# Optimization experiments

Hardware: AMD Instinct MI355X
Metric: run time of the kernel (lower is better)

## Reference

```python
import jax, jax.numpy as jnp
import numpy as np

B, L = 1024, 50
H = 512
N_ITEM, N_ENTITY, N_WORD = 50000, 100000, 30000


def setup_inputs() -> dict:
    key = jax.random.key(0)
    ks = jax.random.split(key, 16)
    inp = {
        "item_ids": jax.random.randint(ks[0], (B, L), 0, N_ITEM),
        "item_len": jax.random.randint(ks[1], (B,), 0, 51),
        "entity_ids": jax.random.randint(ks[2], (B, L), 0, N_ENTITY),
        "entity_len": jax.random.randint(ks[3], (B,), 0, 51),
        "word_ids": jax.random.randint(ks[4], (B, L), 0, N_WORD),
        "word_len": jax.random.randint(ks[5], (B,), 0, 51),
        "labels": jax.random.randint(ks[6], (B,), 0, N_ITEM),
        # learned parameters (torch default-ish init scales)
        "item_emb": jax.random.normal(ks[7], (N_ITEM, H), jnp.float32),
        "entity_emb": jax.random.normal(ks[8], (N_ENTITY, H), jnp.float32),
        "word_emb": jax.random.normal(ks[9], (N_WORD, H), jnp.float32),
        "W1": jax.random.normal(ks[10], (H, 4 * H), jnp.float32) / np.sqrt(H),
        "b1": jnp.zeros((4 * H,), jnp.float32),
        "W2": jax.random.normal(ks[11], (4 * H, N_ITEM), jnp.float32) / np.sqrt(4 * H),
        "b2": jnp.zeros((N_ITEM,), jnp.float32),
    }
    return inp


def _masked_mean(table, ids, lens):
    # segment-mean over ragged lists encoded as padded ids + lengths.
    # empty list -> zeros (matches the torch zero-fallback branch).
    mask = (jnp.arange(L)[None, :] < lens[:, None]).astype(table.dtype)  # [B,L]
    emb = table[ids]                                                     # [B,L,H]
    s = jnp.einsum("blh,bl->bh", emb, mask)
    denom = jnp.maximum(lens, 1).astype(table.dtype)[:, None]
    return s / denom


def reference(item_emb, entity_emb, word_emb, W1, b1, W2, b2,
              item_ids, item_len, entity_ids, entity_len,
              word_ids, word_len, labels):
    u = (_masked_mean(item_emb, item_ids, item_len)
         + _masked_mean(entity_emb, entity_ids, entity_len)
         + _masked_mean(word_emb, word_ids, word_len)) / 3.0   # [B,H]
    h = jax.nn.relu(u @ W1 + b1)                                # [B,4H]
    probs = jax.nn.softmax(h @ W2 + b2, axis=-1)                # [B,n_item]
    # faithful to source: CrossEntropyLoss applied on top of softmax outputs
    logp = jax.nn.log_softmax(probs, axis=-1)
    loss = -jnp.mean(jnp.take_along_axis(logp, labels[:, None], axis=-1))
    return probs, labels, loss
```

## Files before the change

### kernel.cpp

```cpp
#include <hip/hip_runtime.h>
#include <cstdint>
#include <cstddef>

typedef __attribute__((ext_vector_type(8))) short bf16x8;
typedef __attribute__((ext_vector_type(4))) float f32x4;

#define B_DIM 1024
#define L_SEQ 50
#define H_DIM 512
#define NITEM 50000
#define PSTRIDE 400

__device__ __forceinline__ unsigned short f2bf(float x) {
  unsigned u = __float_as_uint(x);
  return (unsigned short)((u + 0x7fffu + ((u >> 16) & 1u)) >> 16);
}
__device__ __forceinline__ unsigned pack2(float lo, float hi) {
  return (unsigned)f2bf(lo) | ((unsigned)f2bf(hi) << 16);
}
__device__ __forceinline__ void gld16(const unsigned short* g, unsigned short* l) {
  __builtin_amdgcn_global_load_lds((const __attribute__((address_space(1))) void*)g,
                                   (__attribute__((address_space(3))) void*)l, 16, 0, 0);
}

__global__ void mean_kernel(const int* __restrict__ item_ids, const int* __restrict__ item_len,
                            const int* __restrict__ ent_ids, const int* __restrict__ ent_len,
                            const int* __restrict__ word_ids, const int* __restrict__ word_len,
                            const float* __restrict__ item_emb, const float* __restrict__ ent_emb,
                            const float* __restrict__ word_emb, unsigned short* __restrict__ u_bf) {
  const int b = blockIdx.x >> 1;
  const int col = ((blockIdx.x & 1) << 8) + threadIdx.x;
  float out = 0.f;
  {
    const int len = item_len[b]; float a = 0.f;
#pragma unroll 4
    for (int l = 0; l < len; ++l) a += item_emb[(size_t)item_ids[b * L_SEQ + l] * H_DIM + col];
    out += a / (float)(len > 0 ? len : 1);
  }
  {
    const int len = ent_len[b]; float a = 0.f;
#pragma unroll 4
    for (int l = 0; l < len; ++l) a += ent_emb[(size_t)ent_ids[b * L_SEQ + l] * H_DIM + col];
    out += a / (float)(len > 0 ? len : 1);
  }
  {
    const int len = word_len[b]; float a = 0.f;
#pragma unroll 4
    for (int l = 0; l < len; ++l) a += word_emb[(size_t)word_ids[b * L_SEQ + l] * H_DIM + col];
    out += a / (float)(len > 0 ? len : 1);
  }
  u_bf[b * H_DIM + col] = f2bf(out / 3.f);
}

template <int K, int N>
__global__ void transpose_bf16(const float* __restrict__ W, unsigned short* __restrict__ Wt) {
  __shared__ float tile[64][65];
  const int k0 = blockIdx.x * 64, n0 = blockIdx.y * 64;
  const int tn = threadIdx.x & 63, tk = threadIdx.x >> 6;
  const int nv = (n0 + tn < N) ? n0 + tn : N - 1;
#pragma unroll
  for (int i = 0; i < 16; ++i)
    tile[tk + 4 * i][tn] = W[(size_t)(k0 + tk + 4 * i) * N + nv];
  __syncthreads();
  const int rn = threadIdx.x >> 2, ck = (threadIdx.x & 3) * 16;
  if (n0 + rn < N) {
    uint4 o[2];
    unsigned* po = (unsigned*)&o[0];
#pragma unroll
    for (int c = 0; c < 8; ++c)
      po[c] = pack2(tile[ck + 2 * c][rn], tile[ck + 2 * c + 1][rn]);
    *(uint4*)&Wt[(size_t)(n0 + rn) * K + k0 + ck] = o[0];
    *(uint4*)&Wt[(size_t)(n0 + rn) * K + k0 + ck + 8] = o[1];
  }
}

template <int K, int N, int EPI>
__global__ __launch_bounds__(512, 2) void gemm_tt(const unsigned short* __restrict__ Ag,
                                                  const unsigned short* __restrict__ Btg,
                                                  const float* __restrict__ bias,
                                                  unsigned short* __restrict__ Cbf,
                                                  float* __restrict__ Cf,
                                                  float* __restrict__ pmax,
                                                  float* __restrict__ psum) {
  __shared__ unsigned short lds[4][2][256 * 32];

  const int tid = threadIdx.x;
  const int lane = tid & 63;
  const int wid = tid >> 6;

  const int nwg = gridDim.x;
  const int xcd = blockIdx.x & 7, off = blockIdx.x >> 3;
  const int q = nwg >> 3, r = nwg & 7;
  const int wgid = (xcd < r ? xcd * (q + 1) : r * (q + 1) + (xcd - r) * q) + off;
  const int m0 = (wgid & 3) * 256;
  const int bn = wgid >> 2;
  const int n0 = bn * 256;

  const int srow = wid * 16 + (lane >> 2);
  const int schunk = lane & 3;
  const unsigned short* pa[2];
  const unsigned short* pb[2];
  unsigned short* da[2];
  unsigned short* db[2];
#pragma unroll
  for (int L = 0; L < 2; ++L) {
    const int row = L * 128 + srow;
    const int cg = schunk ^ ((row >> 1) & 3);
    pa[L] = Ag + (size_t)(m0 + row) * K + cg * 8;
    int rg = n0 + row;
    rg = rg < N ? rg : N - 1;
    pb[L] = Btg + (size_t)rg * K + cg * 8;
    da[L] = &lds[0][0][L * 4096 + wid * 512];
    db[L] = da[L] + 8192;
  }

  auto stage = [&](int t, int s) {
    const int ko = t * 32;
#pragma unroll
    for (int L = 0; L < 2; ++L) gld16(pa[L] + ko, da[L] + s * 16384);
#pragma unroll
    for (int L = 0; L < 2; ++L) gld16(pb[L] + ko, db[L] + s * 16384);
  };

  const int wr = wid >> 2, wc = wid & 3;
  const int l15 = lane & 15, kb = lane >> 4;
  f32x4 acc[8][4] = {};

  auto compute = [&](int s) {
    bf16x8 af[8], bf[4];
#pragma unroll
    for (int i = 0; i < 8; ++i) {
      const int row = wr * 128 + i * 16 + l15;
      const int c = kb ^ ((row >> 1) & 3);
      af[i] = *(const bf16x8*)&lds[s][0][row * 32 + c * 8];
    }
#pragma unroll
    for (int j = 0; j < 4; ++j) {
      const int col = wc * 64 + j * 16 + l15;
      const int c = kb ^ ((col >> 1) & 3);
      bf[j] = *(const bf16x8*)&lds[s][1][col * 32 + c * 8];
    }
    __builtin_amdgcn_s_setprio(1);
#pragma unroll
    for (int i = 0; i < 8; ++i)
#pragma unroll
      for (int j = 0; j < 4; ++j)
        acc[i][j] = __builtin_amdgcn_mfma_f32_16x16x32_bf16(af[i], bf[j], acc[i][j], 0, 0, 0);
    __builtin_amdgcn_s_setprio(0);
  };

  const int NT = K / 32;
  stage(0, 0);
  stage(1, 1);
  asm volatile("s_waitcnt vmcnt(4)" ::: "memory");
  __builtin_amdgcn_sched_barrier(0);
  __builtin_amdgcn_s_barrier();
  __builtin_amdgcn_sched_barrier(0);
  for (int t = 0; t < NT; ++t) {
    if (t + 2 < NT) stage(t + 2, (t + 2) & 3);
    compute(t & 3);
    if (t + 1 < NT) {
      if (t + 2 < NT)
        asm volatile("s_waitcnt vmcnt(4)" ::: "memory");
      else
        asm volatile("s_waitcnt vmcnt(0)" ::: "memory");
      __builtin_amdgcn_sched_barrier(0);
      __builtin_amdgcn_s_barrier();
      __builtin_amdgcn_sched_barrier(0);
    }
  }

  float bv[4];
  bool val[4];
#pragma unroll
  for (int j = 0; j < 4; ++j) {
    const int cg = n0 + wc * 64 + 16 * j + l15;
    val[j] = (cg < N);
    bv[j] = bias[val[j] ? cg : 0];
  }
#pragma unroll
  for (int i = 0; i < 8; ++i) {
    const int rbase = m0 + wr * 128 + 16 * i + 4 * kb;
#pragma unroll
    for (int j = 0; j < 4; ++j) {
      if (val[j]) {
        const int cg = n0 + wc * 64 + 16 * j + l15;
#pragma unroll
        for (int rr = 0; rr < 4; ++rr) {
          const float v = acc[i][j][rr] + bv[j];
          if (EPI == 0)
            Cbf[(size_t)(rbase + rr) * N + cg] = f2bf(v > 0.f ? v : 0.f);
          else
            Cf[(size_t)(rbase + rr) * N + cg] = v;
        }
      }
    }
  }

  if constexpr (EPI == 1) {
    float* redm = (float*)&lds[0][0][0];
    float* reds = redm + 1024;
#pragma unroll
    for (int i = 0; i < 8; ++i) {
#pragma unroll
      for (int rr = 0; rr < 4; ++rr) {
        float mx = -3.0e38f;
#pragma unroll
        for (int j = 0; j < 4; ++j)
          if (val[j]) mx = fmaxf(mx, acc[i][j][rr] + bv[j]);
#pragma unroll
        for (int d = 1; d < 16; d <<= 1) mx = fmaxf(mx, __shfl_xor(mx, d));
        float s = 0.f;
#pragma unroll
        for (int j = 0; j < 4; ++j)
          if (val[j]) s += expf(acc[i][j][rr] + bv[j] - mx);
#pragma unroll
        for (int d = 1; d < 16; d <<= 1) s += __shfl_xor(s, d);
        if (l15 == 0) {
          const int rw = wr * 128 + 16 * i + 4 * kb + rr;
          redm[wc * 256 + rw] = mx;
          reds[wc * 256 + rw] = s;
        }
      }
    }
    __syncthreads();
    if (tid < 256) {
      float mm = redm[tid], ss = reds[tid];
#pragma unroll
      for (int w = 1; w < 4; ++w) {
        const float ma = redm[w * 256 + tid], sa = reds[w * 256 + tid];
        const float nm = fmaxf(mm, ma);
        ss = ss * expf(mm - nm) + sa * expf(ma - nm);
        mm = nm;
      }
      pmax[(size_t)(m0 + tid) * PSTRIDE + bn] = mm;
      psum[(size_t)(m0 + tid) * PSTRIDE + bn] = ss;
    }
  }
}

template <int K, int N, int EPI>
__global__ __launch_bounds__(512, 2) void gemm_fused(const unsigned short* __restrict__ Ag,
                                                     const float* __restrict__ Bg,
                                                     const float* __restrict__ bias,
                                                     unsigned short* __restrict__ Cbf,
                                                     float* __restrict__ Cf,
                                                     float* __restrict__ pmax,
                                                     float* __restrict__ psum) {
  __shared__ unsigned short As[2][256 * 64];
  __shared__ uint4 Bs[2][8 * 128];
  const int tid = threadIdx.x;
  const int lane = tid & 63;
  const int wid = tid >> 6;
  const int m0 = blockIdx.x * 256;
  const int n0 = blockIdx.y * 128;
  const int arow = tid >> 3;
  const int ach = tid & 7;
  const int bn = 2 * lane;
  const int bk = 8 * wid;
  const int bcolg = (n0 + bn < N - 2) ? (n0 + bn) : (N - 2);
  uint4 areg[4];
  float2 breg[8];
  f32x4 acc[4][4] = {};
  auto stage_global = [&](int kt) {
    const int k0 = kt * 64;
#pragma unroll
    for (int qq = 0; qq < 4; ++qq)
      areg[qq] = *(const uint4*)&Ag[(size_t)(m0 + arow + 64 * qq) * K + k0 + 8 * ach];
#pragma unroll
    for (int i = 0; i < 8; ++i) breg[i] = *(const float2*)&Bg[(size_t)(k0 + bk + i) * N + bcolg];
  };
  auto stage_lds = [&](int buf) {
#pragma unroll
    for (int qq = 0; qq < 4; ++qq) {
      const int row = arow + 64 * qq;
      *(uint4*)&As[buf][row * 64 + ((8 * ach) ^ ((row & 7) * 8))] = areg[qq];
    }
    uint4 c0, c1;
    c0.x = pack2(breg[0].x, breg[1].x); c0.y = pack2(breg[2].x, breg[3].x);
    c0.z = pack2(breg[4].x, breg[5].x); c0.w = pack2(breg[6].x, breg[7].x);
    c1.x = pack2(breg[0].y, breg[1].y); c1.y = pack2(breg[2].y, breg[3].y);
    c1.z = pack2(breg[4].y, breg[5].y); c1.w = pack2(breg[6].y, breg[7].y);
    Bs[buf][wid * 128 + bn] = c0;
    Bs[buf][wid * 128 + bn + 1] = c1;
  };
  const int wr = wid & 3, wc = wid >> 2;
  const int mw = 64 * wr, nw = 64 * wc;
  const int l15 = lane & 15, kb = lane >> 4;
  auto compute = [&](int buf) {
#pragma unroll
    for (int koi = 0; koi < 2; ++koi) {
      bf16x8 af[4], bfv[4];
#pragma unroll
      for (int i = 0; i < 4; ++i) {
        const int row = mw + 16 * i + l15;
        af[i] = *(const bf16x8*)&As[buf][row * 64 + ((32 * koi + 8 * kb) ^ ((row & 7) * 8))];
      }
#pragma unroll
      for (int j = 0; j < 4; ++j)
        bfv[j] = *(const bf16x8*)&Bs[buf][(4 * koi + kb) * 128 + nw + 16 * j + l15];
#pragma unroll
      for (int i = 0; i < 4; ++i)
#pragma unroll
        for (int j = 0; j < 4; ++j)
          acc[i][j] = __builtin_amdgcn_mfma_f32_16x16x32_bf16(af[i], bfv[j], acc[i][j], 0, 0, 0);
    }
  };
  const int NT = K / 64;
  stage_global(0);
  stage_lds(0);
  __syncthreads();
  for (int t = 0; t < NT; ++t) {
    const int cur = t & 1;
    if (t + 1 < NT) stage_global(t + 1);
    compute(cur);
    if (t + 1 < NT) stage_lds(cur ^ 1);
    __syncthreads();
  }
  float bv[4];
  bool val[4];
#pragma unroll
  for (int j = 0; j < 4; ++j) {
    const int cg = n0 + nw + 16 * j + l15;
    val[j] = (cg < N);
    bv[j] = bias[val[j] ? cg : 0];
  }
#pragma unroll
  for (int i = 0; i < 4; ++i) {
    const int rbase = m0 + mw + 16 * i + 4 * kb;
#pragma unroll
    for (int j = 0; j < 4; ++j) {
      if (val[j]) {
        const int cg = n0 + nw + 16 * j + l15;
#pragma unroll
        for (int rr = 0; rr < 4; ++rr) {
          const float v = acc[i][j][rr] + bv[j];
          if (EPI == 0)
            Cbf[(size_t)(rbase + rr) * N + cg] = f2bf(v > 0.f ? v : 0.f);
          else
            Cf[(size_t)(rbase + rr) * N + cg] = v;
        }
      }
    }
  }
  if constexpr (EPI == 1) {
    float* redm = (float*)&As[0][0];
    float* reds = redm + 512;
#pragma unroll
    for (int i = 0; i < 4; ++i) {
#pragma unroll
      for (int rr = 0; rr < 4; ++rr) {
        float mx = -3.0e38f;
#pragma unroll
        for (int j = 0; j < 4; ++j)
          if (val[j]) mx = fmaxf(mx, acc[i][j][rr] + bv[j]);
#pragma unroll
        for (int d = 1; d < 16; d <<= 1) mx = fmaxf(mx, __shfl_xor(mx, d));
        float s = 0.f;
#pragma unroll
        for (int j = 0; j < 4; ++j)
          if (val[j]) s += expf(acc[i][j][rr] + bv[j] - mx);
#pragma unroll
        for (int d = 1; d < 16; d <<= 1) s += __shfl_xor(s, d);
        if (l15 == 0) {
          const int rl = mw + 16 * i + 4 * kb + rr;
          redm[wc * 256 + rl] = mx;
          reds[wc * 256 + rl] = s;
        }
      }
    }
    __syncthreads();
    if (tid < 256) {
      const float ma = redm[tid], mb = redm[256 + tid];
      const float mm = fmaxf(ma, mb);
      const float ss = reds[tid] * expf(ma - mm) + reds[256 + tid] * expf(mb - mm);
      pmax[(size_t)(m0 + tid) * PSTRIDE + blockIdx.y] = mm;
      psum[(size_t)(m0 + tid) * PSTRIDE + blockIdx.y] = ss;
    }
  }
}

__global__ void smax1r(const float* __restrict__ pmax, const float* __restrict__ psum,
                       float* __restrict__ rms, int ntiles) {
  const int b = blockIdx.x;
  const int l = threadIdx.x;
  float m = -3.4e38f, s = 0.f;
  for (int i = l; i < ntiles; i += 64) {
    const float pm = pmax[(size_t)b * PSTRIDE + i];
    const float ps = psum[(size_t)b * PSTRIDE + i];
    const float nm = fmaxf(m, pm);
    s = s * expf(m - nm) + ps * expf(pm - nm);
    m = nm;
  }
  for (int d = 1; d < 64; d <<= 1) {
    const float om = __shfl_xor(m, d), os = __shfl_xor(s, d);
    const float nm = fmaxf(m, om);
    s = s * expf(m - nm) + os * expf(om - nm);
    m = nm;
  }
  if (l == 0) {
    rms[b] = m;
    rms[B_DIM + b] = s;
  }
}

__global__ void smax2(float* __restrict__ buf, const float* __restrict__ rms,
                      const int* __restrict__ labels, float* __restrict__ row_lp) {
  const int b = blockIdx.x;
  float4* p = (float4*)(buf + (size_t)b * NITEM);
  const float m = rms[b];
  const float inv = 1.f / rms[B_DIM + b];
  const int lab = labels[b];
  __shared__ float s_pl;
  __shared__ float ss[256];
  float s2 = 0.f;
  for (int i = threadIdx.x; i < NITEM / 4; i += 256) {
    const float4 v = p[i];
    float pr[4];
#pragma unroll
    for (int j = 0; j < 4; ++j) {
      pr[j] = expf((&v.x)[j] - m) * inv;
      s2 += expf(pr[j] - inv);
    }
    float4 w;
    w.x = pr[0]; w.y = pr[1]; w.z = pr[2]; w.w = pr[3];
    p[i] = w;
    if ((lab >> 2) == i) s_pl = pr[lab & 3];
  }
  ss[threadIdx.x] = s2;
  __syncthreads();
  for (int off = 128; off > 0; off >>= 1) {
    if (threadIdx.x < off) ss[threadIdx.x] += ss[threadIdx.x + off];
    __syncthreads();
  }
  if (threadIdx.x == 0) row_lp[b] = s_pl - (inv + logf(ss[0]));
}

__global__ void fin(const float* __restrict__ row_lp, const int* __restrict__ labels,
                    float* __restrict__ out) {
  __shared__ float sb[256];
  float a = 0.f;
  for (int i = threadIdx.x; i < B_DIM; i += 256) {
    a += row_lp[i];
    out[(size_t)B_DIM * NITEM + i] = (float)labels[i];
  }
  sb[threadIdx.x] = a;
  __syncthreads();
  for (int off = 128; off > 0; off >>= 1) {
    if (threadIdx.x < off) sb[threadIdx.x] += sb[threadIdx.x + off];
    __syncthreads();
  }
  if (threadIdx.x == 0) out[(size_t)B_DIM * NITEM + B_DIM] = -sb[0] / (float)B_DIM;
}

extern "C" void kernel_launch(void* const* d_in, const int* in_sizes, int n_in,
                              void* d_out, int out_size, void* d_ws, size_t ws_size,
                              hipStream_t stream) {
  const int* item_ids = (const int*)d_in[0];
  const int* item_len = (const int*)d_in[1];
  const int* ent_ids = (const int*)d_in[2];
  const int* ent_len = (const int*)d_in[3];
  const int* word_ids = (const int*)d_in[4];
  const int* word_len = (const int*)d_in[5];
  const int* labels = (const int*)d_in[6];
  const float* item_emb = (const float*)d_in[7];
  const float* ent_emb = (const float*)d_in[8];
  const float* word_emb = (const float*)d_in[9];
  const float* W1 = (const float*)d_in[10];
  const float* b1 = (const float*)d_in[11];
  const float* W2 = (const float*)d_in[12];
  const float* b2 = (const float*)d_in[13];

  float* out = (float*)d_out;
  char* ws = (char*)d_ws;
  unsigned short* u_bf = (unsigned short*)ws;
  unsigned short* h_bf = (unsigned short*)(ws + (1 << 20));
  float* pmax = (float*)(ws + 5 * (1 << 20));
  float* psum = (float*)(ws + 7 * (1 << 20));
  float* rms = (float*)(ws + 9 * (1 << 20));
  float* row_lp = rms + 2 * B_DIM;
  unsigned short* W1t = (unsigned short*)(ws + 10 * (1 << 20));
  unsigned short* W2t = (unsigned short*)(ws + 16 * (1 << 20));
  float* logits = out;

  const size_t need = (size_t)16 * (1 << 20) + (size_t)NITEM * 2048 * 2;
  const bool fast = ws_size >= need;

  mean_kernel<<<2 * B_DIM, 256, 0, stream>>>(item_ids, item_len, ent_ids, ent_len, word_ids,
                                             word_len, item_emb, ent_emb, word_emb, u_bf);
  if (fast) {
    transpose_bf16<512, 2048><<<dim3(8, 32), 256, 0, stream>>>(W1, W1t);
    transpose_bf16<2048, NITEM><<<dim3(32, 782), 256, 0, stream>>>(W2, W2t);
    gemm_tt<512, 2048, 0><<<4 * 8, 512, 0, stream>>>(u_bf, W1t, b1, h_bf, nullptr, nullptr,
                                                     nullptr);
    gemm_tt<2048, NITEM, 1><<<4 * 196, 512, 0, stream>>>(h_bf, W2t, b2, nullptr, logits, pmax,
                                                         psum);
    smax1r<<<B_DIM, 64, 0, stream>>>(pmax, psum, rms, 196);
  } else {
    gemm_fused<512, 2048, 0><<<dim3(4, 16), 512, 0, stream>>>(u_bf, W1, b1, h_bf, nullptr,
                                                              nullptr, nullptr);
    gemm_fused<2048, NITEM, 1><<<dim3(4, 391), 512, 0, stream>>>(h_bf, W2, b2, nullptr, logits,
                                                                 pmax, psum);
    smax1r<<<B_DIM, 64, 0, stream>>>(pmax, psum, rms, 391);
  }
  smax2<<<B_DIM, 256, 0, stream>>>(logits, rms, labels, row_lp);
  fin<<<1, 256, 0, stream>>>(row_lp, labels, out);
}
```

Before: 587.8 us.

## Deepen GEMM LDS prefetch to three stages and interleave loads with MFMA halves

Restructures the GEMM main loop to keep three k-tiles in flight in a four-slot LDS ring instead of two. Each iteration is split into two MFMA phases, and the A and B global-to-LDS loads for the stage three tiles ahead are issued between them, separated by extra barriers. The vmcnt waits are recomputed from how many stages are outstanding. This is meant to hide global load latency and spread issue pressure, at the cost of more barriers per iteration and an explicit sync before the softmax reduction reuses LDS.

```diff
diff --git a/kernel.cpp b/kernel.cpp
--- a/kernel.cpp
+++ b/kernel.cpp
@@ -82,7 +82,7 @@
                                                   float* __restrict__ Cf,
                                                   float* __restrict__ pmax,
                                                   float* __restrict__ psum) {
-  __shared__ unsigned short lds[4][2][256 * 32];
+  __shared__ unsigned short lds[4 * 16384];
 
   const int tid = threadIdx.x;
   const int lane = tid & 63;
@@ -100,8 +100,6 @@
   const int schunk = lane & 3;
   const unsigned short* pa[2];
   const unsigned short* pb[2];
-  unsigned short* da[2];
-  unsigned short* db[2];
 #pragma unroll
   for (int L = 0; L < 2; ++L) {
     const int row = L * 128 + srow;
@@ -110,64 +108,86 @@
     int rg = n0 + row;
     rg = rg < N ? rg : N - 1;
     pb[L] = Btg + (size_t)rg * K + cg * 8;
-    da[L] = &lds[0][0][L * 4096 + wid * 512];
-    db[L] = da[L] + 8192;
-  }
-
-  auto stage = [&](int t, int s) {
-    const int ko = t * 32;
-#pragma unroll
-    for (int L = 0; L < 2; ++L) gld16(pa[L] + ko, da[L] + s * 16384);
-#pragma unroll
-    for (int L = 0; L < 2; ++L) gld16(pb[L] + ko, db[L] + s * 16384);
-  };
+  }
 
   const int wr = wid >> 2, wc = wid & 3;
   const int l15 = lane & 15, kb = lane >> 4;
   f32x4 acc[8][4] = {};
 
-  auto compute = [&](int s) {
-    bf16x8 af[8], bf[4];
+  const int NT = K / 32;
+#pragma unroll
+  for (int tt = 0; tt < 3; ++tt) {
+    unsigned short* d = &lds[tt * 16384 + wid * 512];
+    const int ko = tt * 32;
+    gld16(pa[0] + ko, d);
+    gld16(pa[1] + ko, d + 4096);
+    gld16(pb[0] + ko, d + 8192);
+    gld16(pb[1] + ko, d + 12288);
+  }
+  asm volatile("s_waitcnt vmcnt(8)" ::: "memory");
+  asm volatile("s_barrier" ::: "memory");
+
+#pragma unroll 1
+  for (int t = 0; t < NT; ++t) {
+    const unsigned short* As_ = &lds[(t & 3) * 16384];
+    const unsigned short* Bs_ = As_ + 8192;
+    unsigned short* ds_ = &lds[((t + 3) & 3) * 16384 + wid * 512];
+    const int kst = (t + 3) * 32;
+    const bool st = (t + 3) < NT;
+
+    bf16x8 af[8];
 #pragma unroll
     for (int i = 0; i < 8; ++i) {
       const int row = wr * 128 + i * 16 + l15;
-      const int c = kb ^ ((row >> 1) & 3);
-      af[i] = *(const bf16x8*)&lds[s][0][row * 32 + c * 8];
-    }
-#pragma unroll
-    for (int j = 0; j < 4; ++j) {
-      const int col = wc * 64 + j * 16 + l15;
-      const int c = kb ^ ((col >> 1) & 3);
-      bf[j] = *(const bf16x8*)&lds[s][1][col * 32 + c * 8];
-    }
+      af[i] = *(const bf16x8*)&As_[row * 32 + (kb ^ ((row >> 1) & 3)) * 8];
+    }
+    bf16x8 b0, b1;
+    {
+      const int c0 = wc * 64 + l15, c1 = c0 + 16;
+      b0 = *(const bf16x8*)&Bs_[c0 * 32 + (kb ^ ((c0 >> 1) & 3)) * 8];
+      b1 = *(const bf16x8*)&Bs_[c1 * 32 + (kb ^ ((c1 >> 1) & 3)) * 8];
+    }
+    if (st) {
+      gld16(pa[0] + kst, ds_);
+      gld16(pa[1] + kst, ds_ + 4096);
+    }
+    asm volatile("s_barrier" ::: "memory");
     __builtin_amdgcn_s_setprio(1);
 #pragma unroll
-    for (int i = 0; i < 8; ++i)
-#pragma unroll
-      for (int j = 0; j < 4; ++j)
-        acc[i][j] = __builtin_amdgcn_mfma_f32_16x16x32_bf16(af[i], bf[j], acc[i][j], 0, 0, 0);
+    for (int i = 0; i < 8; ++i) {
+      acc[i][0] = __builtin_amdgcn_mfma_f32_16x16x32_bf16(af[i], b0, acc[i][0], 0, 0, 0);
+      acc[i][1] = __builtin_amdgcn_mfma_f32_16x16x32_bf16(af[i], b1, acc[i][1], 0, 0, 0);
+    }
     __builtin_amdgcn_s_setprio(0);
-  };
-
-  const int NT = K / 32;
-  stage(0, 0);
-  stage(1, 1);
-  asm volatile("s_waitcnt vmcnt(4)" ::: "memory");
-  __builtin_amdgcn_sched_barrier(0);
-  __builtin_amdgcn_s_barrier();
-  __builtin_amdgcn_sched_barrier(0);
-  for (int t = 0; t < NT; ++t) {
-    if (t + 2 < NT) stage(t + 2, (t + 2) & 3);
-    compute(t & 3);
-    if (t + 1 < NT) {
-      if (t + 2 < NT)
-        asm volatile("s_waitcnt vmcnt(4)" ::: "memory");
-      else
-        asm volatile("s_waitcnt vmcnt(0)" ::: "memory");
-      __builtin_amdgcn_sched_barrier(0);
-      __builtin_amdgcn_s_barrier();
-      __builtin_amdgcn_sched_barrier(0);
-    }
+    asm volatile("s_barrier" ::: "memory");
+
+    bf16x8 b2, b3;
+    {
+      const int c2 = wc * 64 + 32 + l15, c3 = c2 + 16;
+      b2 = *(const bf16x8*)&Bs_[c2 * 32 + (kb ^ ((c2 >> 1) & 3)) * 8];
+      b3 = *(const bf16x8*)&Bs_[c3 * 32 + (kb ^ ((c3 >> 1) & 3)) * 8];
+    }
+    if (st) {
+      gld16(pb[0] + kst, ds_ + 8192);
+      gld16(pb[1] + kst, ds_ + 12288);
+    }
+    asm volatile("s_barrier" ::: "memory");
+    __builtin_amdgcn_s_setprio(1);
+#pragma unroll
+    for (int i = 0; i < 8; ++i) {
+      acc[i][2] = __builtin_amdgcn_mfma_f32_16x16x32_bf16(af[i], b2, acc[i][2], 0, 0, 0);
+      acc[i][3] = __builtin_amdgcn_mfma_f32_16x16x32_bf16(af[i], b3, acc[i][3], 0, 0, 0);
+    }
+    __builtin_amdgcn_s_setprio(0);
+    const int lim = (t + 3 < NT) ? (t + 3) : (NT - 1);
+    const int ahead = lim - (t + 1);
+    if (ahead >= 2)
+      asm volatile("s_waitcnt vmcnt(8)" ::: "memory");
+    else if (ahead == 1)
+      asm volatile("s_waitcnt vmcnt(4)" ::: "memory");
+    else
+      asm volatile("s_waitcnt vmcnt(0)" ::: "memory");
+    asm volatile("s_barrier" ::: "memory");
   }
 
   float bv[4];
@@ -198,7 +218,8 @@
   }
 
   if constexpr (EPI == 1) {
-    float* redm = (float*)&lds[0][0][0];
+    __syncthreads();
+    float* redm = (float*)&lds[0];
     float* reds = redm + 1024;
 #pragma unroll
     for (int i = 0; i < 8; ++i) {
```

Result: no change. 594.0 us (+1.1%).

## Replace 256x256 four-stage GEMM with 128x128 double-buffered tile kernel

Applied to the files above, without the earlier changes.

Swaps the 256x256-tile, 512-thread GEMM (4-stage LDS pipeline, K-step 32, XCD-aware block remap) for a 128x128-tile, 256-thread kernel with K-step 64, double buffering and a plain 2D grid. The aim is more workgroups and better occupancy and load balance across CUs, since the large GEMM goes from 784 to 3128 blocks. The cost is lower data reuse per tile, roughly double the global/L2 traffic for the operands, a shallower prefetch pipeline, and dropping the XCD locality remap. The softmax partials now cover 391 column blocks instead of 196.

```diff
diff --git a/kernel.cpp b/kernel.cpp
--- a/kernel.cpp
+++ b/kernel.cpp
@@ -75,99 +75,84 @@
 }
 
 template <int K, int N, int EPI>
-__global__ __launch_bounds__(512, 2) void gemm_tt(const unsigned short* __restrict__ Ag,
+__global__ __launch_bounds__(256, 2) void gemm128(const unsigned short* __restrict__ Ag,
                                                   const unsigned short* __restrict__ Btg,
                                                   const float* __restrict__ bias,
                                                   unsigned short* __restrict__ Cbf,
                                                   float* __restrict__ Cf,
                                                   float* __restrict__ pmax,
                                                   float* __restrict__ psum) {
-  __shared__ unsigned short lds[4][2][256 * 32];
+  __shared__ unsigned short As[2][128 * 64];
+  __shared__ unsigned short Bs[2][128 * 64];
 
   const int tid = threadIdx.x;
   const int lane = tid & 63;
   const int wid = tid >> 6;
-
-  const int nwg = gridDim.x;
-  const int xcd = blockIdx.x & 7, off = blockIdx.x >> 3;
-  const int q = nwg >> 3, r = nwg & 7;
-  const int wgid = (xcd < r ? xcd * (q + 1) : r * (q + 1) + (xcd - r) * q) + off;
-  const int m0 = (wgid & 3) * 256;
-  const int bn = wgid >> 2;
-  const int n0 = bn * 256;
-
-  const int srow = wid * 16 + (lane >> 2);
-  const int schunk = lane & 3;
-  const unsigned short* pa[2];
-  const unsigned short* pb[2];
-  unsigned short* da[2];
-  unsigned short* db[2];
-#pragma unroll
-  for (int L = 0; L < 2; ++L) {
-    const int row = L * 128 + srow;
-    const int cg = schunk ^ ((row >> 1) & 3);
-    pa[L] = Ag + (size_t)(m0 + row) * K + cg * 8;
+  const int m0 = blockIdx.x * 128;
+  const int n0 = blockIdx.y * 128;
+
+  const int srsub = lane >> 3;
+  const int scg = (lane & 7) ^ srsub;
+  const unsigned short* pa[4];
+  const unsigned short* pb[4];
+#pragma unroll
+  for (int qq = 0; qq < 4; ++qq) {
+    const int seg = wid * 4 + qq;
+    const int row = seg * 8 + srsub;
+    pa[qq] = Ag + (size_t)(m0 + row) * K + scg * 8;
     int rg = n0 + row;
     rg = rg < N ? rg : N - 1;
-    pb[L] = Btg + (size_t)rg * K + cg * 8;
-    da[L] = &lds[0][0][L * 4096 + wid * 512];
-    db[L] = da[L] + 8192;
+    pb[qq] = Btg + (size_t)rg * K + scg * 8;
   }
 
   auto stage = [&](int t, int s) {
-    const int ko = t * 32;
-#pragma unroll
-    for (int L = 0; L < 2; ++L) gld16(pa[L] + ko, da[L] + s * 16384);
-#pragma unroll
-    for (int L = 0; L < 2; ++L) gld16(pb[L] + ko, db[L] + s * 16384);
+    const int ko = t * 64;
+#pragma unroll
+    for (int qq = 0; qq < 4; ++qq) {
+      const int seg = wid * 4 + qq;
+      gld16(pa[qq] + ko, &As[s][seg * 512]);
+      gld16(pb[qq] + ko, &Bs[s][seg * 512]);
+    }
   };
 
-  const int wr = wid >> 2, wc = wid & 3;
+  const int wr = wid >> 1, wc = wid & 1;
   const int l15 = lane & 15, kb = lane >> 4;
-  f32x4 acc[8][4] = {};
+  f32x4 acc[4][4] = {};
 
   auto compute = [&](int s) {
-    bf16x8 af[8], bf[4];
-#pragma unroll
-    for (int i = 0; i < 8; ++i) {
-      const int row = wr * 128 + i * 16 + l15;
-      const int c = kb ^ ((row >> 1) & 3);
-      af[i] = *(const bf16x8*)&lds[s][0][row * 32 + c * 8];
-    }
-#pragma unroll
-    for (int j = 0; j < 4; ++j) {
-      const int col = wc * 64 + j * 16 + l15;
-      const int c = kb ^ ((col >> 1) & 3);
-      bf[j] = *(const bf16x8*)&lds[s][1][col * 32 + c * 8];
-    }
-    __builtin_amdgcn_s_setprio(1);
-#pragma unroll
-    for (int i = 0; i < 8; ++i)
-#pragma unroll
-      for (int j = 0; j < 4; ++j)
-        acc[i][j] = __builtin_amdgcn_mfma_f32_16x16x32_bf16(af[i], bf[j], acc[i][j], 0, 0, 0);
-    __builtin_amdgcn_s_setprio(0);
+#pragma unroll
+    for (int koi = 0; koi < 2; ++koi) {
+      bf16x8 af[4], bf[4];
+#pragma unroll
+      for (int i = 0; i < 4; ++i) {
+        const int row = wr * 64 + i * 16 + l15;
+        const int c = (koi * 4 + kb) ^ (row & 7);
+        af[i] = *(const bf16x8*)&As[s][row * 64 + c * 8];
+      }
+#pragma unroll
+      for (int j = 0; j < 4; ++j) {
+        const int col = wc * 64 + j * 16 + l15;
+        const int c = (koi * 4 + kb) ^ (col & 7);
+        bf[j] = *(const bf16x8*)&Bs[s][col * 64 + c * 8];
+      }
+#pragma unroll
+      for (int i = 0; i < 4; ++i)
+#pragma unroll
+        for (int j = 0; j < 4; ++j)
+          acc[i][j] = __builtin_amdgcn_mfma_f32_16x16x32_bf16(af[i], bf[j], acc[i][j], 0, 0, 0);
+    }
   };
 
-  const int NT = K / 32;
+  const int NT = K / 64;
   stage(0, 0);
-  stage(1, 1);
-  asm volatile("s_waitcnt vmcnt(4)" ::: "memory");
-  __builtin_amdgcn_sched_barrier(0);
-  __builtin_amdgcn_s_barrier();
-  __builtin_amdgcn_sched_barrier(0);
+  asm volatile("s_waitcnt vmcnt(0)" ::: "memory");
+  __syncthreads();
+#pragma unroll 1
   for (int t = 0; t < NT; ++t) {
-    if (t + 2 < NT) stage(t + 2, (t + 2) & 3);
-    compute(t & 3);
-    if (t + 1 < NT) {
-      if (t + 2 < NT)
-        asm volatile("s_waitcnt vmcnt(4)" ::: "memory");
-      else
-        asm volatile("s_waitcnt vmcnt(0)" ::: "memory");
-      __builtin_amdgcn_sched_barrier(0);
-      __builtin_amdgcn_s_barrier();
-      __builtin_amdgcn_sched_barrier(0);
-    }
+    if (t + 1 < NT) stage(t + 1, (t + 1) & 1);
+    compute(t & 1);
+    asm volatile("s_waitcnt vmcnt(0)" ::: "memory");
+    __syncthreads();
   }
 
   float bv[4];
@@ -179,8 +164,8 @@
     bv[j] = bias[val[j] ? cg : 0];
   }
 #pragma unroll
-  for (int i = 0; i < 8; ++i) {
-    const int rbase = m0 + wr * 128 + 16 * i + 4 * kb;
+  for (int i = 0; i < 4; ++i) {
+    const int rbase = m0 + wr * 64 + 16 * i + 4 * kb;
 #pragma unroll
     for (int j = 0; j < 4; ++j) {
       if (val[j]) {
@@ -198,10 +183,10 @@
   }
 
   if constexpr (EPI == 1) {
-    float* redm = (float*)&lds[0][0][0];
-    float* reds = redm + 1024;
-#pragma unroll
-    for (int i = 0; i < 8; ++i) {
+    float* redm = (float*)&As[0][0];
+    float* reds = redm + 256;
+#pragma unroll
+    for (int i = 0; i < 4; ++i) {
 #pragma unroll
       for (int rr = 0; rr < 4; ++rr) {
         float mx = -3.0e38f;
@@ -217,24 +202,19 @@
 #pragma unroll
         for (int d = 1; d < 16; d <<= 1) s += __shfl_xor(s, d);
         if (l15 == 0) {
-          const int rw = wr * 128 + 16 * i + 4 * kb + rr;
-          redm[wc * 256 + rw] = mx;
-          reds[wc * 256 + rw] = s;
+          const int rw = wr * 64 + 16 * i + 4 * kb + rr;
+          redm[wc * 128 + rw] = mx;
+          reds[wc * 128 + rw] = s;
         }
       }
     }
     __syncthreads();
-    if (tid < 256) {
-      float mm = redm[tid], ss = reds[tid];
-#pragma unroll
-      for (int w = 1; w < 4; ++w) {
-        const float ma = redm[w * 256 + tid], sa = reds[w * 256 + tid];
-        const float nm = fmaxf(mm, ma);
-        ss = ss * expf(mm - nm) + sa * expf(ma - nm);
-        mm = nm;
-      }
-      pmax[(size_t)(m0 + tid) * PSTRIDE + bn] = mm;
-      psum[(size_t)(m0 + tid) * PSTRIDE + bn] = ss;
+    if (tid < 128) {
+      const float ma = redm[tid], mb = redm[128 + tid];
+      const float mm = fmaxf(ma, mb);
+      const float ss = reds[tid] * expf(ma - mm) + reds[128 + tid] * expf(mb - mm);
+      pmax[(size_t)(m0 + tid) * PSTRIDE + blockIdx.y] = mm;
+      psum[(size_t)(m0 + tid) * PSTRIDE + blockIdx.y] = ss;
     }
   }
 }
@@ -491,11 +471,11 @@
   if (fast) {
     transpose_bf16<512, 2048><<<dim3(8, 32), 256, 0, stream>>>(W1, W1t);
     transpose_bf16<2048, NITEM><<<dim3(32, 782), 256, 0, stream>>>(W2, W2t);
-    gemm_tt<512, 2048, 0><<<4 * 8, 512, 0, stream>>>(u_bf, W1t, b1, h_bf, nullptr, nullptr,
-                                                     nullptr);
-    gemm_tt<2048, NITEM, 1><<<4 * 196, 512, 0, stream>>>(h_bf, W2t, b2, nullptr, logits, pmax,
-                                                         psum);
-    smax1r<<<B_DIM, 64, 0, stream>>>(pmax, psum, rms, 196);
+    gemm128<512, 2048, 0><<<dim3(8, 16), 256, 0, stream>>>(u_bf, W1t, b1, h_bf, nullptr,
+                                                           nullptr, nullptr);
+    gemm128<2048, NITEM, 1><<<dim3(8, 391), 256, 0, stream>>>(h_bf, W2t, b2, nullptr, logits,
+                                                              pmax, psum);
+    smax1r<<<B_DIM, 64, 0, stream>>>(pmax, psum, rms, 391);
   } else {
     gemm_fused<512, 2048, 0><<<dim3(4, 16), 512, 0, stream>>>(u_bf, W1, b1, h_bf, nullptr,
                                                               nullptr, nullptr);
```

New measurement: 661.4 us. 12.5% more time.
